# Kernel tuning notes

Hardware: AMD Instinct MI355X
Metric: run time of the kernel (lower is better)

Reference implementation:

```python
import jax, jax.numpy as jnp
import numpy as np

N_NODES = 100000


def gcn_conv(x, edge_index, W, b):
    """PyG GCNConv: add self-loops, symmetric deg^{-1/2} normalization,
    linear transform, scatter-add aggregation, then bias."""
    n = x.shape[0]
    loops = jnp.arange(n, dtype=edge_index.dtype)
    src = jnp.concatenate([edge_index[0], loops])  # [E+N]
    dst = jnp.concatenate([edge_index[1], loops])  # [E+N]
    # degree (with self-loops) of each target node
    deg = jax.ops.segment_sum(jnp.ones_like(dst, dtype=x.dtype), dst, num_segments=n)
    dinv = jnp.where(deg > 0, jax.lax.rsqrt(deg), 0.0)
    norm = dinv[src] * dinv[dst]  # [E+N]
    h = x @ W  # [N, out_dim] -- transform before aggregation
    msg = h[src] * norm[:, None]  # gather + normalize
    out = jax.ops.segment_sum(msg, dst, num_segments=n)  # scatter-add
    return out + b


def setup_inputs() -> dict:
    key = jax.random.key(0)
    ks = jax.random.split(key, 8)
    n, e, d_in, d_h = N_NODES, 1600000, 32, 64
    x = jax.random.normal(ks[0], (n, d_in), dtype=jnp.float32)
    edge_index = jax.random.randint(ks[1], (2, e), 0, n, dtype=jnp.int64)
    # Glorot-style init for GCN weights, uniform for linear layer
    W1 = jax.random.normal(ks[2], (d_in, d_h), dtype=jnp.float32) / np.sqrt(d_in)
    b1 = jnp.zeros((d_h,), dtype=jnp.float32)
    W2 = jax.random.normal(ks[3], (d_h, d_h), dtype=jnp.float32) / np.sqrt(d_h)
    b2 = jnp.zeros((d_h,), dtype=jnp.float32)
    Wo = jax.random.normal(ks[4], (d_h, 1), dtype=jnp.float32) / np.sqrt(d_h)
    bo = jnp.zeros((1,), dtype=jnp.float32)
    return {"x": x, "edge_index": edge_index, "W1": W1, "b1": b1,
            "W2": W2, "b2": b2, "Wo": Wo, "bo": bo}


def reference(x, edge_index, W1, b1, W2, b2, Wo, bo):
    h = jax.nn.relu(gcn_conv(x, edge_index, W1, b1))
    h = jax.nn.relu(gcn_conv(h, edge_index, W2, b2))
    logits = h @ Wo + bo  # [N, 1]
    return jax.nn.sigmoid(logits).squeeze(-1)  # [N]
```

## Files before the change

### kernel.cpp

```cpp
#include <hip/hip_runtime.h>

#define DH 64
#define DIN 32
#define BSH 8
#define BNODES 256
#define MAXB 1024
#define CAPSH 13
#define CAP (1 << CAPSH)

typedef unsigned short u16;
typedef unsigned int u32;

__device__ __forceinline__ float bf2f(u16 u) {
    union { u32 i; float f; } x; x.i = ((u32)u) << 16; return x.f;
}
__device__ __forceinline__ u16 f2bf(float f) {
    union { float f; u32 i; } x; x.f = f;
    u32 r = x.i + 0x7fff + ((x.i >> 16) & 1);
    return (u16)(r >> 16);
}

__global__ void __launch_bounds__(256) binA_k(
        const int* __restrict__ ei, int* __restrict__ gcnt,
        u32* __restrict__ pairs, int E, int n, int nbuck) {
    __shared__ int lhist[MAXB];
    __shared__ int lbase[MAXB];
    __shared__ int smode;
    int t = threadIdx.x;
    if (t < 64) {
        int v = (2 * t + 1 < 2 * E) ? ei[2 * t + 1] : 0;
        unsigned long long b = __ballot(v != 0);
        if (t == 0) smode = (b != 0ULL) ? 1 : 0;
    }
    for (int b = t; b < nbuck; b += 256) lhist[b] = 0;
    __syncthreads();
    int m = smode;
    unsigned un = (unsigned)n;
    int q0 = blockIdx.x * 256 + t;
    int qs = gridDim.x * 256;

    if (m && !(E & 3)) {
        const int4* d4 = (const int4*)(ei + E);
        for (int q = q0; q < (E >> 2); q += qs) {
            int4 d = d4[q];
            if ((unsigned)d.x < un) atomicAdd(&lhist[d.x >> BSH], 1);
            if ((unsigned)d.y < un) atomicAdd(&lhist[d.y >> BSH], 1);
            if ((unsigned)d.z < un) atomicAdd(&lhist[d.z >> BSH], 1);
            if ((unsigned)d.w < un) atomicAdd(&lhist[d.w >> BSH], 1);
        }
    } else if (!m && !(E & 1)) {
        const int4* d4 = (const int4*)(ei + 2 * E);
        for (int q = q0; q < (E >> 1); q += qs) {
            int4 d = d4[q];
            if ((unsigned)d.x < un) atomicAdd(&lhist[d.x >> BSH], 1);
            if ((unsigned)d.z < un) atomicAdd(&lhist[d.z >> BSH], 1);
        }
    } else {
        const int* dstp = m ? (ei + E) : (ei + 2 * E);
        int stride = m ? 1 : 2;
        for (int e = q0; e < E; e += qs) {
            int d = dstp[(size_t)e * stride];
            if ((unsigned)d < un) atomicAdd(&lhist[d >> BSH], 1);
        }
    }
    __syncthreads();
    for (int b = t; b < nbuck; b += 256) {
        int c = lhist[b];
        lbase[b] = c ? ((b << CAPSH) + atomicAdd(&gcnt[b], c)) : 0;
        lhist[b] = 0;
    }
    __syncthreads();
    #define EMIT(S, D)                                                     \
        if ((unsigned)(D) < un) {                                          \
            int sv = ((unsigned)(S) < un) ? (S) : 0;                       \
            int bb = (D) >> BSH;                                           \
            int off = atomicAdd(&lhist[bb], 1);                            \
            int pos = lbase[bb] + off;                                     \
            if (pos < ((bb + 1) << CAPSH))                                 \
                pairs[pos] = ((u32)sv << BSH) | (u32)((D) & (BNODES - 1)); \
        }
    if (m && !(E & 3)) {
        const int4* s4 = (const int4*)ei;
        const int4* d4 = (const int4*)(ei + E);
        for (int q = q0; q < (E >> 2); q += qs) {
            int4 s = s4[q]; int4 d = d4[q];
            EMIT(s.x, d.x) EMIT(s.y, d.y) EMIT(s.z, d.z) EMIT(s.w, d.w)
        }
    } else if (!m && !(E & 1)) {
        const int4* s4 = (const int4*)ei;
        const int4* d4 = (const int4*)(ei + 2 * E);
        for (int q = q0; q < (E >> 1); q += qs) {
            int4 s = s4[q]; int4 d = d4[q];
            EMIT(s.x, d.x) EMIT(s.z, d.z)
        }
    } else {
        const int* srcp = ei;
        const int* dstp = m ? (ei + E) : (ei + 2 * E);
        int stride = m ? 1 : 2;
        for (int e = q0; e < E; e += qs) {
            int d = dstp[(size_t)e * stride];
            int s = srcp[(size_t)e * stride];
            EMIT(s, d)
        }
    }
    #undef EMIT
}

__global__ void __launch_bounds__(512) csr_gemm_k(
        u32* __restrict__ pairs, const int* __restrict__ gcnt,
        int* __restrict__ rstart, int* __restrict__ rend,
        int* __restrict__ col, float* __restrict__ dinv,
        const float* __restrict__ x, const float* __restrict__ W1, int N) {
    __shared__ int cnt[BNODES];
    __shared__ int s[BNODES];
    __shared__ float dl[BNODES];
    __shared__ float Wl[DIN * DH];
    __shared__ float xl[32][DIN + 4];
    int b = blockIdx.x, t = threadIdx.x;
    int base = b << CAPSH;
    int ec = gcnt[b]; if (ec > CAP) ec = CAP;
    int end = base + ec;
    ((float4*)Wl)[t] = ((const float4*)W1)[t];
    if (t < BNODES) cnt[t] = 0;
    __syncthreads();
    for (int i = base + t; i < end; i += 512)
        atomicAdd(&cnt[pairs[i] & (BNODES - 1)], 1);
    __syncthreads();
    int v = (t < BNODES) ? cnt[t] : 0;
    if (t < BNODES) s[t] = v;
    __syncthreads();
    for (int off = 1; off < BNODES; off <<= 1) {
        int xsc = (t >= off && t < BNODES) ? s[t - off] : 0;
        __syncthreads();
        if (t < BNODES) s[t] += xsc;
        __syncthreads();
    }
    if (t < BNODES) {
        int excl = s[t] - v;
        int a = base + excl;
        int node = (b << BSH) + t;
        float di = rsqrtf((float)v + 1.0f);
        dl[t] = di;
        if (node < N) {
            rstart[node] = a;
            rend[node]   = a + v;
            dinv[node]   = di;
        }
        cnt[t] = a;
    }
    __syncthreads();
    for (int i = base + t; i < end; i += 512) {
        u32 p = pairs[i];
        int pos = atomicAdd(&cnt[p & (BNODES - 1)], 1);
        col[pos] = (int)(p >> BSH);
    }
    __syncthreads();
    u16* hp = (u16*)pairs;
    int lane = t & 63, w = t >> 6;
    int g = lane >> 4, c = lane & 15;
    for (int it = 0; it < 8; it++) {
        int nl0 = it * 32;
        __syncthreads();
        if (t < 256) {
            int idx = t * 4;
            int row = idx / DIN, ck = idx % DIN;
            int node = (b << BSH) + nl0 + row;
            float4 vx = {0.f, 0.f, 0.f, 0.f};
            if (node < N)
                vx = *(const float4*)&x[(size_t)node * DIN + ck];
            *(float4*)&xl[row][ck] = vx;
        }
        __syncthreads();
        int nl = nl0 + w * 4 + g;
        int node = (b << BSH) + nl;
        const float* xr = xl[nl - nl0];
        float4 acc = {0.f, 0.f, 0.f, 0.f};
        #pragma unroll
        for (int k = 0; k < DIN; k++) {
            float xv = xr[k];
            float4 wv = *(const float4*)&Wl[k * DH + c * 4];
            acc.x += xv * wv.x; acc.y += xv * wv.y; acc.z += xv * wv.z; acc.w += xv * wv.w;
        }
        if (node < N) {
            float di = dl[nl];
            ushort4 o;
            o.x = f2bf(acc.x * di); o.y = f2bf(acc.y * di);
            o.z = f2bf(acc.z * di); o.w = f2bf(acc.w * di);
            *(ushort4*)&hp[(size_t)node * DH + c * 4] = o;
        }
    }
}

__device__ __forceinline__ float4 edge_sum_grp(const u16* __restrict__ hp,
                                               const int* __restrict__ col,
                                               int start, int deg, int g, int c) {
    int dm = deg;
    dm = max(dm, __shfl_xor(dm, 16, 64));
    dm = max(dm, __shfl_xor(dm, 32, 64));
    float4 acc = {0.f, 0.f, 0.f, 0.f};
    if (dm <= 0) return acc;
    int gl = g << 4;
    int cb = (c < deg) ? col[start + c] : 0;
    for (int base = 0; base < dm; base += 16) {
        int nb = base + 16;
        int cbn = 0;
        if (nb < dm) cbn = (nb + c < deg) ? col[start + nb + c] : 0;
        int rm = dm - base; if (rm > 16) rm = 16;
        for (int j = 0; j < rm; j += 8) {
            int s0 = __shfl(cb, gl | j, 64);
            int s1 = __shfl(cb, gl | (j + 1), 64);
            int s2 = __shfl(cb, gl | (j + 2), 64);
            int s3 = __shfl(cb, gl | (j + 3), 64);
            int s4 = __shfl(cb, gl | (j + 4), 64);
            int s5 = __shfl(cb, gl | (j + 5), 64);
            int s6 = __shfl(cb, gl | (j + 6), 64);
            int s7 = __shfl(cb, gl | (j + 7), 64);
            bool a0 = base + j     < deg;
            bool a1 = base + j + 1 < deg;
            bool a2 = base + j + 2 < deg;
            bool a3 = base + j + 3 < deg;
            bool a4 = base + j + 4 < deg;
            bool a5 = base + j + 5 < deg;
            bool a6 = base + j + 6 < deg;
            bool a7 = base + j + 7 < deg;
            ushort4 v0, v1, v2, v3, v4, v5, v6, v7;
            if (a0) v0 = *(const ushort4*)&hp[(size_t)s0 * DH + c * 4];
            if (a1) v1 = *(const ushort4*)&hp[(size_t)s1 * DH + c * 4];
            if (a2) v2 = *(const ushort4*)&hp[(size_t)s2 * DH + c * 4];
            if (a3) v3 = *(const ushort4*)&hp[(size_t)s3 * DH + c * 4];
            if (a4) v4 = *(const ushort4*)&hp[(size_t)s4 * DH + c * 4];
            if (a5) v5 = *(const ushort4*)&hp[(size_t)s5 * DH + c * 4];
            if (a6) v6 = *(const ushort4*)&hp[(size_t)s6 * DH + c * 4];
            if (a7) v7 = *(const ushort4*)&hp[(size_t)s7 * DH + c * 4];
            if (a0) { acc.x += bf2f(v0.x); acc.y += bf2f(v0.y); acc.z += bf2f(v0.z); acc.w += bf2f(v0.w); }
            if (a1) { acc.x += bf2f(v1.x); acc.y += bf2f(v1.y); acc.z += bf2f(v1.z); acc.w += bf2f(v1.w); }
            if (a2) { acc.x += bf2f(v2.x); acc.y += bf2f(v2.y); acc.z += bf2f(v2.z); acc.w += bf2f(v2.w); }
            if (a3) { acc.x += bf2f(v3.x); acc.y += bf2f(v3.y); acc.z += bf2f(v3.z); acc.w += bf2f(v3.w); }
            if (a4) { acc.x += bf2f(v4.x); acc.y += bf2f(v4.y); acc.z += bf2f(v4.z); acc.w += bf2f(v4.w); }
            if (a5) { acc.x += bf2f(v5.x); acc.y += bf2f(v5.y); acc.z += bf2f(v5.z); acc.w += bf2f(v5.w); }
            if (a6) { acc.x += bf2f(v6.x); acc.y += bf2f(v6.y); acc.z += bf2f(v6.z); acc.w += bf2f(v6.w); }
            if (a7) { acc.x += bf2f(v7.x); acc.y += bf2f(v7.y); acc.z += bf2f(v7.z); acc.w += bf2f(v7.w); }
        }
        cb = cbn;
    }
    return acc;
}

__global__ void __launch_bounds__(256) agg_gemm_k(
        const u16* __restrict__ hp, const int* __restrict__ rstart,
        const int* __restrict__ rend, const int* __restrict__ col,
        const float* __restrict__ dinv, const float* __restrict__ b1,
        const float* __restrict__ W2, u16* __restrict__ hp2, int N) {
    __shared__ float Wl[DH * DH];
    __shared__ float xs[4][4][DH + 4];
    int tid = threadIdx.x;
    {
        const float4* Wv = (const float4*)W2;
        float4* Wd = (float4*)Wl;
        #pragma unroll
        for (int r = 0; r < 4; r++) Wd[tid + 256 * r] = Wv[tid + 256 * r];
    }
    __syncthreads();
    int lane = tid & 63, w = tid >> 6;
    int g = lane >> 4, c = lane & 15;
    int node = blockIdx.x * 16 + w * 4 + g;
    int start = 0, deg = 0;
    if (node < N) { start = rstart[node]; deg = rend[node] - start; }
    float4 acc = edge_sum_grp(hp, col, start, deg, g, c);
    float di = (node < N) ? dinv[node] : 0.f;
    float4 o = {0.f, 0.f, 0.f, 0.f};
    if (node < N) {
        ushort4 sv = *(const ushort4*)&hp[(size_t)node * DH + c * 4];
        float4 b = *(const float4*)&b1[c * 4];
        o.x = fmaxf((acc.x + bf2f(sv.x)) * di + b.x, 0.f);
        o.y = fmaxf((acc.y + bf2f(sv.y)) * di + b.y, 0.f);
        o.z = fmaxf((acc.z + bf2f(sv.z)) * di + b.z, 0.f);
        o.w = fmaxf((acc.w + bf2f(sv.w)) * di + b.w, 0.f);
    }
    *(float4*)&xs[w][g][c * 4] = o;
    const float* xr = xs[w][g];
    float4 a2 = {0.f, 0.f, 0.f, 0.f};
    #pragma unroll
    for (int k = 0; k < DH; k++) {
        float xv = xr[k];
        float4 wv = *(const float4*)&Wl[k * DH + c * 4];
        a2.x += xv * wv.x; a2.y += xv * wv.y; a2.z += xv * wv.z; a2.w += xv * wv.w;
    }
    if (node < N) {
        ushort4 po;
        po.x = f2bf(a2.x * di); po.y = f2bf(a2.y * di);
        po.z = f2bf(a2.z * di); po.w = f2bf(a2.w * di);
        *(ushort4*)&hp2[(size_t)node * DH + c * 4] = po;
    }
}

__global__ void __launch_bounds__(256) agg_head_k(
        const u16* __restrict__ hp, const int* __restrict__ rstart,
        const int* __restrict__ rend, const int* __restrict__ col,
        const float* __restrict__ dinv, const float* __restrict__ bias,
        const float* __restrict__ Wo, const float* __restrict__ bo,
        float* __restrict__ y, int N) {
    int lane = threadIdx.x & 63;
    int g = lane >> 4, c = lane & 15;
    int node = blockIdx.x * 16 + (threadIdx.x >> 6) * 4 + g;
    int start = 0, deg = 0;
    if (node < N) { start = rstart[node]; deg = rend[node] - start; }
    float4 acc = edge_sum_grp(hp, col, start, deg, g, c);
    float t = 0.f;
    if (node < N) {
        ushort4 sv = *(const ushort4*)&hp[(size_t)node * DH + c * 4];
        float4 b = *(const float4*)&bias[c * 4];
        float4 wo = *(const float4*)&Wo[c * 4];
        float di = dinv[node];
        t = fmaxf((acc.x + bf2f(sv.x)) * di + b.x, 0.f) * wo.x
          + fmaxf((acc.y + bf2f(sv.y)) * di + b.y, 0.f) * wo.y
          + fmaxf((acc.z + bf2f(sv.z)) * di + b.z, 0.f) * wo.z
          + fmaxf((acc.w + bf2f(sv.w)) * di + b.w, 0.f) * wo.w;
    }
    #pragma unroll
    for (int m = 1; m < 16; m <<= 1) t += __shfl_xor(t, m, 64);
    if (c == 0 && node < N) {
        float z = t + bo[0];
        y[node] = 1.f / (1.f + __expf(-z));
    }
}

extern "C" void kernel_launch(void* const* d_in, const int* in_sizes, int n_in,
                              void* d_out, int out_size, void* d_ws, size_t ws_size,
                              hipStream_t stream) {
    const float* x  = (const float*)d_in[0];
    const int*   ei = (const int*)d_in[1];
    const float* W1 = (const float*)d_in[2];
    const float* b1 = (const float*)d_in[3];
    const float* W2 = (const float*)d_in[4];
    const float* b2 = (const float*)d_in[5];
    const float* Wo = (const float*)d_in[6];
    const float* bo = (const float*)d_in[7];
    float* y = (float*)d_out;

    int N = in_sizes[0] / DIN;
    int E = in_sizes[1] / 2;
    int nbuck = ((N - 1) >> BSH) + 1;

    char* ws = (char*)d_ws;
    size_t off = 0;
    auto alloc = [&](size_t bytes) { char* p = ws + off; off += (bytes + 255) & ~(size_t)255; return p; };
    int*   gcnt   = (int*)alloc(MAXB * 4);
    int*   rstart = (int*)alloc((size_t)N * 4);
    int*   rend   = (int*)alloc((size_t)N * 4);
    float* dinv   = (float*)alloc((size_t)N * 4);
    int*   col    = (int*)alloc(((size_t)nbuck << CAPSH) * 4);
    size_t pair_b = ((size_t)nbuck << CAPSH) * 4;
    size_t hp_b   = (size_t)N * DH * 2;
    char*  bufA   = (char*)alloc(pair_b > hp_b ? pair_b : hp_b);
    u16*   bufB   = (u16*)alloc(hp_b);
    u16*   hp    = (u16*)bufA;
    u32*   pairs = (u32*)bufA;

    int gN16 = (N + 15) / 16;

    hipMemsetAsync(gcnt, 0, (size_t)nbuck * 4, stream);
    binA_k<<<768, 256, 0, stream>>>(ei, gcnt, pairs, E, N, nbuck);
    csr_gemm_k<<<nbuck, 512, 0, stream>>>(pairs, gcnt, rstart, rend, col, dinv, x, W1, N);
    agg_gemm_k<<<gN16, 256, 0, stream>>>(hp, rstart, rend, col, dinv, b1, W2, bufB, N);
    agg_head_k<<<gN16, 256, 0, stream>>>(bufB, rstart, rend, col, dinv, b2, Wo, bo, y, N);
}
```

Measured before the change: 199.4 us.

## Widen edge gather to 16B per lane with 8-lane node groups and sentinel row

Restructures the neighbor aggregation so each node is handled by 8 lanes loading 16-byte chunks instead of 16 lanes loading 8-byte chunks, doubling nodes per block. Out-of-range edges now point at a zeroed sentinel row appended after each feature buffer, which removes the per-edge predication. Accumulation uses packed v_pk_add_f32 on bf16 pairs. This cuts instruction and branch overhead in the gather loop, at the cost of extra workspace and more registers per lane.

```diff
diff --git a/kernel.cpp b/kernel.cpp
--- a/kernel.cpp
+++ b/kernel.cpp
@@ -10,6 +10,7 @@
 
 typedef unsigned short u16;
 typedef unsigned int u32;
+typedef float f32x2 __attribute__((ext_vector_type(2)));
 
 __device__ __forceinline__ float bf2f(u16 u) {
     union { u32 i; float f; } x; x.i = ((u32)u) << 16; return x.f;
@@ -18,6 +19,17 @@
     union { float f; u32 i; } x; x.f = f;
     u32 r = x.i + 0x7fff + ((x.i >> 16) & 1);
     return (u16)(r >> 16);
+}
+__device__ __forceinline__ float bfl(u32 u) {
+    union { u32 i; float f; } x; x.i = u << 16; return x.f;
+}
+__device__ __forceinline__ float bfh(u32 u) {
+    union { u32 i; float f; } x; x.i = u & 0xffff0000u; return x.f;
+}
+__device__ __forceinline__ void pkacc(f32x2& a, u32 u) {
+    f32x2 b;
+    b[0] = bfl(u); b[1] = bfh(u);
+    asm("v_pk_add_f32 %0, %1, %0" : "+v"(a) : "v"(b));
 }
 
 __global__ void __launch_bounds__(256) binA_k(
@@ -189,61 +201,53 @@
             *(ushort4*)&hp[(size_t)node * DH + c * 4] = o;
         }
     }
-}
-
-__device__ __forceinline__ float4 edge_sum_grp(const u16* __restrict__ hp,
-                                               const int* __restrict__ col,
-                                               int start, int deg, int g, int c) {
+    if (b == 0 && t < 32)
+        ((float*)((char*)pairs + (size_t)N * DH * 2))[t] = 0.f;
+}
+
+__device__ __forceinline__ void edge_sum8(const u16* __restrict__ hp,
+                                          const int* __restrict__ col,
+                                          int start, int deg, int g, int c,
+                                          int nsent, f32x2* __restrict__ acc) {
     int dm = deg;
+    dm = max(dm, __shfl_xor(dm, 8, 64));
     dm = max(dm, __shfl_xor(dm, 16, 64));
     dm = max(dm, __shfl_xor(dm, 32, 64));
-    float4 acc = {0.f, 0.f, 0.f, 0.f};
-    if (dm <= 0) return acc;
-    int gl = g << 4;
-    int cb = (c < deg) ? col[start + c] : 0;
-    for (int base = 0; base < dm; base += 16) {
-        int nb = base + 16;
-        int cbn = 0;
-        if (nb < dm) cbn = (nb + c < deg) ? col[start + nb + c] : 0;
-        int rm = dm - base; if (rm > 16) rm = 16;
-        for (int j = 0; j < rm; j += 8) {
-            int s0 = __shfl(cb, gl | j, 64);
-            int s1 = __shfl(cb, gl | (j + 1), 64);
-            int s2 = __shfl(cb, gl | (j + 2), 64);
-            int s3 = __shfl(cb, gl | (j + 3), 64);
-            int s4 = __shfl(cb, gl | (j + 4), 64);
-            int s5 = __shfl(cb, gl | (j + 5), 64);
-            int s6 = __shfl(cb, gl | (j + 6), 64);
-            int s7 = __shfl(cb, gl | (j + 7), 64);
-            bool a0 = base + j     < deg;
-            bool a1 = base + j + 1 < deg;
-            bool a2 = base + j + 2 < deg;
-            bool a3 = base + j + 3 < deg;
-            bool a4 = base + j + 4 < deg;
-            bool a5 = base + j + 5 < deg;
-            bool a6 = base + j + 6 < deg;
-            bool a7 = base + j + 7 < deg;
-            ushort4 v0, v1, v2, v3, v4, v5, v6, v7;
-            if (a0) v0 = *(const ushort4*)&hp[(size_t)s0 * DH + c * 4];
-            if (a1) v1 = *(const ushort4*)&hp[(size_t)s1 * DH + c * 4];
-            if (a2) v2 = *(const ushort4*)&hp[(size_t)s2 * DH + c * 4];
-            if (a3) v3 = *(const ushort4*)&hp[(size_t)s3 * DH + c * 4];
-            if (a4) v4 = *(const ushort4*)&hp[(size_t)s4 * DH + c * 4];
-            if (a5) v5 = *(const ushort4*)&hp[(size_t)s5 * DH + c * 4];
-            if (a6) v6 = *(const ushort4*)&hp[(size_t)s6 * DH + c * 4];
-            if (a7) v7 = *(const ushort4*)&hp[(size_t)s7 * DH + c * 4];
-            if (a0) { acc.x += bf2f(v0.x); acc.y += bf2f(v0.y); acc.z += bf2f(v0.z); acc.w += bf2f(v0.w); }
-            if (a1) { acc.x += bf2f(v1.x); acc.y += bf2f(v1.y); acc.z += bf2f(v1.z); acc.w += bf2f(v1.w); }
-            if (a2) { acc.x += bf2f(v2.x); acc.y += bf2f(v2.y); acc.z += bf2f(v2.z); acc.w += bf2f(v2.w); }
-            if (a3) { acc.x += bf2f(v3.x); acc.y += bf2f(v3.y); acc.z += bf2f(v3.z); acc.w += bf2f(v3.w); }
-            if (a4) { acc.x += bf2f(v4.x); acc.y += bf2f(v4.y); acc.z += bf2f(v4.z); acc.w += bf2f(v4.w); }
-            if (a5) { acc.x += bf2f(v5.x); acc.y += bf2f(v5.y); acc.z += bf2f(v5.z); acc.w += bf2f(v5.w); }
-            if (a6) { acc.x += bf2f(v6.x); acc.y += bf2f(v6.y); acc.z += bf2f(v6.z); acc.w += bf2f(v6.w); }
-            if (a7) { acc.x += bf2f(v7.x); acc.y += bf2f(v7.y); acc.z += bf2f(v7.z); acc.w += bf2f(v7.w); }
-        }
+    if (dm <= 0) return;
+    int gl = g << 3;
+    u32 co = (u32)c << 4;
+    const char* hpb = (const char*)hp;
+    int cb = (c < deg) ? col[start + c] : nsent;
+    for (int base = 0; base < dm; base += 8) {
+        int nb = base + 8;
+        int cbn = nsent;
+        if (nb < dm) cbn = (nb + c < deg) ? col[start + nb + c] : nsent;
+        int s0 = __shfl(cb, gl | 0, 64);
+        int s1 = __shfl(cb, gl | 1, 64);
+        int s2 = __shfl(cb, gl | 2, 64);
+        int s3 = __shfl(cb, gl | 3, 64);
+        int s4 = __shfl(cb, gl | 4, 64);
+        int s5 = __shfl(cb, gl | 5, 64);
+        int s6 = __shfl(cb, gl | 6, 64);
+        int s7 = __shfl(cb, gl | 7, 64);
+        uint4 v0 = *(const uint4*)(hpb + ((((u32)s0) << 7) | co));
+        uint4 v1 = *(const uint4*)(hpb + ((((u32)s1) << 7) | co));
+        uint4 v2 = *(const uint4*)(hpb + ((((u32)s2) << 7) | co));
+        uint4 v3 = *(const uint4*)(hpb + ((((u32)s3) << 7) | co));
+        uint4 v4 = *(const uint4*)(hpb + ((((u32)s4) << 7) | co));
+        uint4 v5 = *(const uint4*)(hpb + ((((u32)s5) << 7) | co));
+        uint4 v6 = *(const uint4*)(hpb + ((((u32)s6) << 7) | co));
+        uint4 v7 = *(const uint4*)(hpb + ((((u32)s7) << 7) | co));
+        pkacc(acc[0], v0.x); pkacc(acc[1], v0.y); pkacc(acc[2], v0.z); pkacc(acc[3], v0.w);
+        pkacc(acc[0], v1.x); pkacc(acc[1], v1.y); pkacc(acc[2], v1.z); pkacc(acc[3], v1.w);
+        pkacc(acc[0], v2.x); pkacc(acc[1], v2.y); pkacc(acc[2], v2.z); pkacc(acc[3], v2.w);
+        pkacc(acc[0], v3.x); pkacc(acc[1], v3.y); pkacc(acc[2], v3.z); pkacc(acc[3], v3.w);
+        pkacc(acc[0], v4.x); pkacc(acc[1], v4.y); pkacc(acc[2], v4.z); pkacc(acc[3], v4.w);
+        pkacc(acc[0], v5.x); pkacc(acc[1], v5.y); pkacc(acc[2], v5.z); pkacc(acc[3], v5.w);
+        pkacc(acc[0], v6.x); pkacc(acc[1], v6.y); pkacc(acc[2], v6.z); pkacc(acc[3], v6.w);
+        pkacc(acc[0], v7.x); pkacc(acc[1], v7.y); pkacc(acc[2], v7.z); pkacc(acc[3], v7.w);
         cb = cbn;
     }
-    return acc;
 }
 
 __global__ void __launch_bounds__(256) agg_gemm_k(
@@ -252,7 +256,7 @@
         const float* __restrict__ dinv, const float* __restrict__ b1,
         const float* __restrict__ W2, u16* __restrict__ hp2, int N) {
     __shared__ float Wl[DH * DH];
-    __shared__ float xs[4][4][DH + 4];
+    __shared__ float xs[4][8][DH + 4];
     int tid = threadIdx.x;
     {
         const float4* Wv = (const float4*)W2;
@@ -260,37 +264,56 @@
         #pragma unroll
         for (int r = 0; r < 4; r++) Wd[tid + 256 * r] = Wv[tid + 256 * r];
     }
+    if (blockIdx.x == 0 && tid < 32)
+        ((float*)(hp2 + (size_t)N * DH))[tid] = 0.f;
     __syncthreads();
     int lane = tid & 63, w = tid >> 6;
-    int g = lane >> 4, c = lane & 15;
-    int node = blockIdx.x * 16 + w * 4 + g;
+    int g = lane >> 3, c = lane & 7;
+    int node = blockIdx.x * 32 + w * 8 + g;
     int start = 0, deg = 0;
     if (node < N) { start = rstart[node]; deg = rend[node] - start; }
-    float4 acc = edge_sum_grp(hp, col, start, deg, g, c);
+    f32x2 acc[4] = {{0.f,0.f},{0.f,0.f},{0.f,0.f},{0.f,0.f}};
+    edge_sum8(hp, col, start, deg, g, c, N, acc);
     float di = (node < N) ? dinv[node] : 0.f;
-    float4 o = {0.f, 0.f, 0.f, 0.f};
+    float o0=0.f,o1=0.f,o2=0.f,o3=0.f,o4=0.f,o5=0.f,o6=0.f,o7=0.f;
     if (node < N) {
-        ushort4 sv = *(const ushort4*)&hp[(size_t)node * DH + c * 4];
-        float4 b = *(const float4*)&b1[c * 4];
-        o.x = fmaxf((acc.x + bf2f(sv.x)) * di + b.x, 0.f);
-        o.y = fmaxf((acc.y + bf2f(sv.y)) * di + b.y, 0.f);
-        o.z = fmaxf((acc.z + bf2f(sv.z)) * di + b.z, 0.f);
-        o.w = fmaxf((acc.w + bf2f(sv.w)) * di + b.w, 0.f);
-    }
-    *(float4*)&xs[w][g][c * 4] = o;
+        uint4 sv = *(const uint4*)&hp[(size_t)node * DH + c * 8];
+        float4 blo = *(const float4*)&b1[c * 8];
+        float4 bhi = *(const float4*)&b1[c * 8 + 4];
+        o0 = fmaxf((acc[0][0] + bfl(sv.x)) * di + blo.x, 0.f);
+        o1 = fmaxf((acc[0][1] + bfh(sv.x)) * di + blo.y, 0.f);
+        o2 = fmaxf((acc[1][0] + bfl(sv.y)) * di + blo.z, 0.f);
+        o3 = fmaxf((acc[1][1] + bfh(sv.y)) * di + blo.w, 0.f);
+        o4 = fmaxf((acc[2][0] + bfl(sv.z)) * di + bhi.x, 0.f);
+        o5 = fmaxf((acc[2][1] + bfh(sv.z)) * di + bhi.y, 0.f);
+        o6 = fmaxf((acc[3][0] + bfl(sv.w)) * di + bhi.z, 0.f);
+        o7 = fmaxf((acc[3][1] + bfh(sv.w)) * di + bhi.w, 0.f);
+    }
+    *(float4*)&xs[w][g][c * 8]     = make_float4(o0, o1, o2, o3);
+    *(float4*)&xs[w][g][c * 8 + 4] = make_float4(o4, o5, o6, o7);
     const float* xr = xs[w][g];
-    float4 a2 = {0.f, 0.f, 0.f, 0.f};
+    float4 alo = {0.f,0.f,0.f,0.f}, ahi = {0.f,0.f,0.f,0.f};
     #pragma unroll
-    for (int k = 0; k < DH; k++) {
-        float xv = xr[k];
-        float4 wv = *(const float4*)&Wl[k * DH + c * 4];
-        a2.x += xv * wv.x; a2.y += xv * wv.y; a2.z += xv * wv.z; a2.w += xv * wv.w;
+    for (int k4 = 0; k4 < DH / 4; k4++) {
+        float4 xv4 = *(const float4*)&xr[k4 * 4];
+        float xj[4] = {xv4.x, xv4.y, xv4.z, xv4.w};
+        #pragma unroll
+        for (int j = 0; j < 4; j++) {
+            const float* wr = &Wl[(k4 * 4 + j) * DH + c * 8];
+            float4 w0 = *(const float4*)wr;
+            float4 w1 = *(const float4*)(wr + 4);
+            float xv = xj[j];
+            alo.x += xv * w0.x; alo.y += xv * w0.y; alo.z += xv * w0.z; alo.w += xv * w0.w;
+            ahi.x += xv * w1.x; ahi.y += xv * w1.y; ahi.z += xv * w1.z; ahi.w += xv * w1.w;
+        }
     }
     if (node < N) {
-        ushort4 po;
-        po.x = f2bf(a2.x * di); po.y = f2bf(a2.y * di);
-        po.z = f2bf(a2.z * di); po.w = f2bf(a2.w * di);
-        *(ushort4*)&hp2[(size_t)node * DH + c * 4] = po;
+        uint4 po;
+        po.x = (u32)f2bf(alo.x * di) | ((u32)f2bf(alo.y * di) << 16);
+        po.y = (u32)f2bf(alo.z * di) | ((u32)f2bf(alo.w * di) << 16);
+        po.z = (u32)f2bf(ahi.x * di) | ((u32)f2bf(ahi.y * di) << 16);
+        po.w = (u32)f2bf(ahi.z * di) | ((u32)f2bf(ahi.w * di) << 16);
+        *(uint4*)&hp2[(size_t)node * DH + c * 8] = po;
     }
 }
 
@@ -301,24 +324,32 @@
         const float* __restrict__ Wo, const float* __restrict__ bo,
         float* __restrict__ y, int N) {
     int lane = threadIdx.x & 63;
-    int g = lane >> 4, c = lane & 15;
-    int node = blockIdx.x * 16 + (threadIdx.x >> 6) * 4 + g;
+    int g = lane >> 3, c = lane & 7;
+    int node = blockIdx.x * 32 + (threadIdx.x >> 6) * 8 + g;
     int start = 0, deg = 0;
     if (node < N) { start = rstart[node]; deg = rend[node] - start; }
-    float4 acc = edge_sum_grp(hp, col, start, deg, g, c);
+    f32x2 acc[4] = {{0.f,0.f},{0.f,0.f},{0.f,0.f},{0.f,0.f}};
+    edge_sum8(hp, col, start, deg, g, c, N, acc);
     float t = 0.f;
     if (node < N) {
-        ushort4 sv = *(const ushort4*)&hp[(size_t)node * DH + c * 4];
-        float4 b = *(const float4*)&bias[c * 4];
-        float4 wo = *(const float4*)&Wo[c * 4];
+        uint4 sv = *(const uint4*)&hp[(size_t)node * DH + c * 8];
+        float4 blo = *(const float4*)&bias[c * 8];
+        float4 bhi = *(const float4*)&bias[c * 8 + 4];
+        float4 wlo = *(const float4*)&Wo[c * 8];
+        float4 whi = *(const float4*)&Wo[c * 8 + 4];
         float di = dinv[node];
-        t = fmaxf((acc.x + bf2f(sv.x)) * di + b.x, 0.f) * wo.x
-          + fmaxf((acc.y + bf2f(sv.y)) * di + b.y, 0.f) * wo.y
-          + fmaxf((acc.z + bf2f(sv.z)) * di + b.z, 0.f) * wo.z
-          + fmaxf((acc.w + bf2f(sv.w)) * di + b.w, 0.f) * wo.w;
-    }
-    #pragma unroll
-    for (int m = 1; m < 16; m <<= 1) t += __shfl_xor(t, m, 64);
+        t = fmaxf((acc[0][0] + bfl(sv.x)) * di + blo.x, 0.f) * wlo.x
+          + fmaxf((acc[0][1] + bfh(sv.x)) * di + blo.y, 0.f) * wlo.y
+          + fmaxf((acc[1][0] + bfl(sv.y)) * di + blo.z, 0.f) * wlo.z
+          + fmaxf((acc[1][1] + bfh(sv.y)) * di + blo.w, 0.f) * wlo.w
+          + fmaxf((acc[2][0] + bfl(sv.z)) * di + bhi.x, 0.f) * whi.x
+          + fmaxf((acc[2][1] + bfh(sv.z)) * di + bhi.y, 0.f) * whi.y
+          + fmaxf((acc[3][0] + bfl(sv.w)) * di + bhi.z, 0.f) * whi.z
+          + fmaxf((acc[3][1] + bfh(sv.w)) * di + bhi.w, 0.f) * whi.w;
+    }
+    t += __shfl_xor(t, 1, 64);
+    t += __shfl_xor(t, 2, 64);
+    t += __shfl_xor(t, 4, 64);
     if (c == 0 && node < N) {
         float z = t + bo[0];
         y[node] = 1.f / (1.f + __expf(-z));
@@ -351,17 +382,17 @@
     float* dinv   = (float*)alloc((size_t)N * 4);
     int*   col    = (int*)alloc(((size_t)nbuck << CAPSH) * 4);
     size_t pair_b = ((size_t)nbuck << CAPSH) * 4;
-    size_t hp_b   = (size_t)N * DH * 2;
+    size_t hp_b   = (size_t)N * DH * 2 + 256;
     char*  bufA   = (char*)alloc(pair_b > hp_b ? pair_b : hp_b);
     u16*   bufB   = (u16*)alloc(hp_b);
     u16*   hp    = (u16*)bufA;
     u32*   pairs = (u32*)bufA;
 
-    int gN16 = (N + 15) / 16;
+    int gN32 = (N + 31) / 32;
 
     hipMemsetAsync(gcnt, 0, (size_t)nbuck * 4, stream);
     binA_k<<<768, 256, 0, stream>>>(ei, gcnt, pairs, E, N, nbuck);
     csr_gemm_k<<<nbuck, 512, 0, stream>>>(pairs, gcnt, rstart, rend, col, dinv, x, W1, N);
-    agg_gemm_k<<<gN16, 256, 0, stream>>>(hp, rstart, rend, col, dinv, b1, W2, bufB, N);
-    agg_head_k<<<gN16, 256, 0, stream>>>(bufB, rstart, rend, col, dinv, b2, Wo, bo, y, N);
-}
+    agg_gemm_k<<<gN32, 256, 0, stream>>>(hp, rstart, rend, col, dinv, b1, W2, bufB, N);
+    agg_head_k<<<gN32, 256, 0, stream>>>(bufB, rstart, rend, col, dinv, b2, Wo, bo, y, N);
+}
```

After: 199.0 us. About the same (-0.2%).
